# Kernel tuning notes

Measured on AMD Instinct MI355X. Metric: run time of the kernel, lower is better.

Reference implementation:

```python
import jax, jax.numpy as jnp
import numpy as np

WS = 7      # window size
NH = 16     # num heads
DIM = 512
B, H, W = 128, 28, 28


def _relative_position_index(ws):
    coords = np.stack(np.meshgrid(np.arange(ws), np.arange(ws), indexing='ij'))  # [2,ws,ws]
    coords = coords.reshape(2, -1)                                               # [2,ws^2]
    rel = coords[:, :, None] - coords[:, None, :]                                # [2,ws^2,ws^2]
    rel = rel.transpose(1, 2, 0)
    rel[:, :, 0] += ws - 1
    rel[:, :, 1] += ws - 1
    rel[:, :, 0] *= 2 * ws - 1
    return rel.sum(-1).reshape(-1).astype(np.int32)                              # [ws^2*ws^2]


def setup_inputs() -> dict:
    key = jax.random.key(0)
    ks = jax.random.split(key, 6)
    x = jax.random.normal(ks[0], (B, H, W, DIM), dtype=jnp.float32)
    nW = (H // WS) * (W // WS)
    mask = jnp.zeros((nW, WS * WS, WS * WS), dtype=jnp.float32)  # shifted-window mask (zeros = no shift)
    w_qkv = jax.random.normal(ks[1], (DIM, 3 * DIM), dtype=jnp.float32) * (DIM ** -0.5)
    b_qkv = jnp.zeros((3 * DIM,), dtype=jnp.float32)
    bias_table = jax.random.normal(ks[2], ((2 * WS - 1) ** 2, NH), dtype=jnp.float32) * 0.02
    w_proj = jax.random.normal(ks[3], (DIM, DIM), dtype=jnp.float32) * (DIM ** -0.5)
    b_proj = jnp.zeros((DIM,), dtype=jnp.float32)
    rel_index = jnp.asarray(_relative_position_index(WS))
    return {"x": x, "mask": mask, "w_qkv": w_qkv, "b_qkv": b_qkv,
            "bias_table": bias_table, "w_proj": w_proj, "b_proj": b_proj,
            "rel_index": rel_index, "height": H, "width": W}


def reference(x, mask, w_qkv, b_qkv, bias_table, w_proj, b_proj, rel_index, height, width):
    Bc, Hc, Wc, C = x.shape
    ws, nh = WS, NH
    hd = C // nh
    scale = hd ** -0.5
    hW, wW = height // ws, width // ws
    nW = hW * wW
    L = ws * ws

    # QKV projection: [B,H,W,3C]
    qkv = x @ w_qkv + b_qkv
    # fused window partition -> [3, B*nW, nh, ws^2, hd]
    qkv = qkv.reshape(Bc, hW, ws, wW, ws, 3, nh, hd)
    qkv = qkv.transpose(5, 0, 1, 3, 6, 2, 4, 7).reshape(3, Bc * nW, nh, L, hd)
    q, k, v = qkv[0], qkv[1], qkv[2]

    # scaled dot-product scores per window
    attn = jnp.einsum('wnqd,wnkd->wnqk', q * scale, k)  # [B*nW, nh, L, L]
    # relative position bias gather: [L*L, nh] -> [nh, L, L]
    bias = bias_table[rel_index].reshape(L, L, nh).transpose(2, 0, 1)
    attn = attn + bias[None]
    # shifted-window attention mask
    attn = attn.reshape(Bc, nW, nh, L, L) + mask[None, :, None]
    attn = jax.nn.softmax(attn, axis=-1).reshape(Bc * nW, nh, L, L)

    out = jnp.einsum('wnqk,wnkd->wnqd', attn, v)  # [B*nW, nh, L, hd]
    # fused window reverse -> [B,H,W,C]
    out = out.reshape(Bc, hW, wW, nh, ws, ws, hd)
    out = out.transpose(0, 1, 4, 2, 5, 3, 6).reshape(Bc, height, width, C)
    return out @ w_proj + b_proj
```

## Files before the change

### kernel.cpp

```cpp
#include <hip/hip_runtime.h>
#include <hip/hip_bf16.h>
#include <stdint.h>

typedef __bf16 bf16_t;
typedef bf16_t bf16x8 __attribute__((ext_vector_type(8)));
typedef float f32x4 __attribute__((ext_vector_type(4)));

#define MFMA16(a, b, c) __builtin_amdgcn_mfma_f32_16x16x32_bf16(a, b, c, 0, 0, 0)

static constexpr float kScale = 0.17677669529663687f;
static constexpr int CROWS = 25088;
static constexpr int NCHUNK = 4;

__device__ __forceinline__ void gload16(const bf16_t* g, bf16_t* l) {
  __builtin_amdgcn_global_load_lds(
      (const __attribute__((address_space(1))) unsigned int*)g,
      (__attribute__((address_space(3))) unsigned int*)l, 16, 0, 0);
}

__global__ __launch_bounds__(256) void k_prep(
    const float* __restrict__ wqkv,
    const float* __restrict__ wproj,
    const float* __restrict__ btab,
    const float* __restrict__ mask,
    const int*   __restrict__ relidx,
    bf16_t* __restrict__ wqkvT,
    bf16_t* __restrict__ wprojT,
    float*  __restrict__ bmm)
{
  int idx = blockIdx.x * 256 + threadIdx.x;
  if (idx < 1536 * 512) {
    int n = idx >> 9, k = idx & 511;
    wqkvT[idx] = (bf16_t)wqkv[k * 1536 + n];
  } else if (idx < 1536 * 512 + 512 * 512) {
    int t = idx - 1536 * 512;
    int n = t >> 9, k = t & 511;
    wprojT[t] = (bf16_t)wproj[k * 512 + n];
  } else if (idx < 1536 * 512 + 512 * 512 + 16 * 16 * 49 * 49) {
    int t = idx - (1536 * 512 + 512 * 512);
    int j = t % 49;  int t2 = t / 49;
    int i = t2 % 49; int t3 = t2 / 49;
    int h = t3 & 15; int wi = t3 >> 4;
    bmm[t] = btab[relidx[i * 49 + j] * 16 + h] + mask[(wi * 49 + i) * 49 + j];
  }
}

__global__ __launch_bounds__(256) void k_cvt(
    const float* __restrict__ x, bf16_t* __restrict__ xb)
{
  size_t i = (size_t)(blockIdx.x * 256 + threadIdx.x) * 8;
  float4 f0 = *(const float4*)(x + i);
  float4 f1 = *(const float4*)(x + i + 4);
  bf16x8 v;
  v[0] = (bf16_t)f0.x; v[1] = (bf16_t)f0.y; v[2] = (bf16_t)f0.z; v[3] = (bf16_t)f0.w;
  v[4] = (bf16_t)f1.x; v[5] = (bf16_t)f1.y; v[6] = (bf16_t)f1.z; v[7] = (bf16_t)f1.w;
  *(bf16x8*)(xb + i) = v;
}

template<int LDA, int NLD, bool ISQKV>
__global__ __launch_bounds__(256) void k_gemm(
    const bf16_t* __restrict__ A,
    const bf16_t* __restrict__ Bmat,
    const float*  __restrict__ bias,
    bf16_t* __restrict__ outb,
    float*  __restrict__ outf)
{
  __shared__ alignas(16) bf16_t As[128 * 64];
  __shared__ alignas(16) bf16_t Bs[128 * 64];
  const int tid  = threadIdx.x;
  const int wv   = tid >> 6, lane = tid & 63;
  const int quad = lane >> 4, l16 = lane & 15;
  const int nt0 = blockIdx.x * 128, mt0 = blockIdx.y * 128;
  const int wr = (wv >> 1) * 64, wc = (wv & 1) * 64;

  const int rsub = lane >> 3;
  const int colp = ((lane & 7) ^ rsub) * 8;
  const bf16_t* ga = A    + (size_t)(mt0 + wv * 32 + rsub) * LDA + colp;
  const bf16_t* gb = Bmat + (size_t)(nt0 + wv * 32 + rsub) * 512 + colp;
  bf16_t* lA = As + wv * 32 * 64;
  bf16_t* lB = Bs + wv * 32 * 64;

  const f32x4 z4 = {0.f, 0.f, 0.f, 0.f};
  f32x4 acc[4][4];
#pragma unroll
  for (int a = 0; a < 4; ++a)
#pragma unroll
    for (int b = 0; b < 4; ++b) acc[a][b] = z4;

  for (int kt = 0; kt < 8; ++kt) {
    const int k0 = kt * 64;
#pragma unroll
    for (int c = 0; c < 4; ++c) {
      gload16(ga + (size_t)c * 8 * LDA + k0, lA + c * 512);
      gload16(gb + c * 8 * 512 + k0, lB + c * 512);
    }
    __syncthreads();
#pragma unroll
    for (int kk = 0; kk < 2; ++kk) {
      bf16x8 af[4], bfr[4];
#pragma unroll
      for (int mt = 0; mt < 4; ++mt) {
        int row = wr + mt * 16 + l16;
        af[mt] = *(const bf16x8*)&As[row * 64 + ((kk * 32 + quad * 8) ^ ((l16 & 7) * 8))];
      }
#pragma unroll
      for (int nt = 0; nt < 4; ++nt) {
        int row = wc + nt * 16 + l16;
        bfr[nt] = *(const bf16x8*)&Bs[row * 64 + ((kk * 32 + quad * 8) ^ ((l16 & 7) * 8))];
      }
#pragma unroll
      for (int mt = 0; mt < 4; ++mt)
#pragma unroll
        for (int nt = 0; nt < 4; ++nt)
          acc[mt][nt] = MFMA16(af[mt], bfr[nt], acc[mt][nt]);
    }
    __syncthreads();
  }

#pragma unroll
  for (int nt = 0; nt < 4; ++nt) {
    int col = nt0 + wc + nt * 16 + l16;
    float bv = bias[col];
#pragma unroll
    for (int mt = 0; mt < 4; ++mt) {
#pragma unroll
      for (int r = 0; r < 4; ++r) {
        size_t row = (size_t)(mt0 + wr + mt * 16 + quad * 4 + r);
        float v = acc[mt][nt][r] + bv;
        if constexpr (ISQKV) {
          if (col < 512) v *= kScale;
          outb[row * NLD + col] = (bf16_t)v;
        } else {
          outf[row * NLD + col] = v;
        }
      }
    }
  }
}

__global__ __launch_bounds__(256) void k_attn2(
    bf16_t* __restrict__ qkv,
    const float* __restrict__ bmm)
{
  __shared__ alignas(16) bf16_t lds[4 * 6144];
  const int tid  = threadIdx.x;
  const int wv   = tid >> 6, lane = tid & 63;
  const int quad = lane >> 4, l16 = lane & 15;
  const int h = blockIdx.x * 4 + wv;
  const int w = blockIdx.y;
  const int bimg = w >> 4, wi = w & 15;
  const int rowbase = bimg * 784 + (wi >> 2) * 196 + (wi & 3) * 7;
  char* ps  = (char*)(lds + wv * 6144);
  char* vts = (char*)(lds + wv * 6144 + 4096);

  for (int u = lane; u < 32 * 16; u += 64) {
    int d = u >> 4, j = 48 + (u & 15);
    *(bf16_t*)(vts + ((d * 128 + j * 2) ^ ((d & 7) << 4))) = (bf16_t)0.f;
  }
  const bf16_t* vbase = qkv + 1024 + h * 32;
  for (int u = lane; u < 49 * 4; u += 64) {
    int l = u >> 2, dg = u & 3;
    size_t r = (size_t)(rowbase + (l / 7) * 28 + (l % 7));
    bf16x8 vvv = *(const bf16x8*)(vbase + r * 1536 + dg * 8);
#pragma unroll
    for (int e = 0; e < 8; ++e) {
      int d = dg * 8 + e;
      *(bf16_t*)(vts + ((d * 128 + l * 2) ^ ((d & 7) << 4))) = vvv[e];
    }
  }

  const bf16_t* qbase = qkv + h * 32;
  const bf16_t* kbase = qkv + 512 + h * 32;
  const f32x4 z4 = {0.f, 0.f, 0.f, 0.f};
  f32x4 sacc[4][4];
#pragma unroll
  for (int a = 0; a < 4; ++a)
#pragma unroll
    for (int b = 0; b < 4; ++b) sacc[a][b] = z4;

  bf16x8 kb[4];
#pragma unroll
  for (int nt = 0; nt < 4; ++nt) {
    int t = nt * 16 + l16; if (t > 48) t = 48;
    size_t r = (size_t)(rowbase + (t / 7) * 28 + (t % 7));
    kb[nt] = *(const bf16x8*)(kbase + r * 1536 + quad * 8);
  }
#pragma unroll
  for (int mt = 0; mt < 4; ++mt) {
    int t = mt * 16 + l16; if (t > 48) t = 48;
    size_t r = (size_t)(rowbase + (t / 7) * 28 + (t % 7));
    bf16x8 qa = *(const bf16x8*)(qbase + r * 1536 + quad * 8);
#pragma unroll
    for (int nt = 0; nt < 4; ++nt) sacc[mt][nt] = MFMA16(qa, kb[nt], sacc[mt][nt]);
  }

  const float* bm = bmm + (wi * 16 + h) * 2401;
#pragma unroll
  for (int mt = 0; mt < 4; ++mt) {
#pragma unroll
    for (int rr = 0; rr < 4; ++rr) {
      int i = mt * 16 + quad * 4 + rr;
      bool iv = (i < 49);
      float sv[4], mx = -3e38f;
#pragma unroll
      for (int nt = 0; nt < 4; ++nt) {
        int j = nt * 16 + l16;
        sv[nt] = (iv && j < 49) ? (sacc[mt][nt][rr] + bm[i * 49 + j]) : -3e38f;
        mx = fmaxf(mx, sv[nt]);
      }
#pragma unroll
      for (int off = 1; off < 16; off <<= 1) mx = fmaxf(mx, __shfl_xor(mx, off, 16));
      float ex[4], sum = 0.f;
#pragma unroll
      for (int nt = 0; nt < 4; ++nt) {
        ex[nt] = (sv[nt] > -2e38f) ? __expf(sv[nt] - mx) : 0.f;
        sum += ex[nt];
      }
#pragma unroll
      for (int off = 1; off < 16; off <<= 1) sum += __shfl_xor(sum, off, 16);
      float rinv = (sum > 0.f) ? (1.f / sum) : 0.f;
#pragma unroll
      for (int nt = 0; nt < 4; ++nt) {
        int j = nt * 16 + l16;
        *(bf16_t*)(ps + ((i * 128 + j * 2) ^ ((i & 7) << 4))) = (bf16_t)(ex[nt] * rinv);
      }
    }
  }

  asm volatile("" ::: "memory");

  f32x4 oacc[4][2];
#pragma unroll
  for (int a = 0; a < 4; ++a) { oacc[a][0] = z4; oacc[a][1] = z4; }
#pragma unroll
  for (int kk = 0; kk < 2; ++kk) {
    bf16x8 vb[2];
#pragma unroll
    for (int nt = 0; nt < 2; ++nt) {
      int d = nt * 16 + l16;
      vb[nt] = *(const bf16x8*)(vts + ((d * 128 + (kk * 32 + quad * 8) * 2) ^ ((d & 7) << 4)));
    }
#pragma unroll
    for (int mt = 0; mt < 4; ++mt) {
      int i = mt * 16 + l16;
      bf16x8 pa = *(const bf16x8*)(ps + ((i * 128 + (kk * 32 + quad * 8) * 2) ^ ((i & 7) << 4)));
#pragma unroll
      for (int nt = 0; nt < 2; ++nt) oacc[mt][nt] = MFMA16(pa, vb[nt], oacc[mt][nt]);
    }
  }

  bf16_t* obase = qkv + h * 32;
#pragma unroll
  for (int mt = 0; mt < 4; ++mt) {
#pragma unroll
    for (int rr = 0; rr < 4; ++rr) {
      int l = mt * 16 + quad * 4 + rr;
      if (l < 49) {
        size_t r = (size_t)(rowbase + (l / 7) * 28 + (l % 7));
#pragma unroll
        for (int nt = 0; nt < 2; ++nt)
          obase[r * 1536 + nt * 16 + l16] = (bf16_t)oacc[mt][nt][rr];
      }
    }
  }
}

extern "C" void kernel_launch(void* const* d_in, const int* in_sizes, int n_in,
                              void* d_out, int out_size, void* d_ws, size_t ws_size,
                              hipStream_t stream) {
  const float* x     = (const float*)d_in[0];
  const float* mask  = (const float*)d_in[1];
  const float* wqkv  = (const float*)d_in[2];
  const float* bqkv  = (const float*)d_in[3];
  const float* btab  = (const float*)d_in[4];
  const float* wproj = (const float*)d_in[5];
  const float* bproj = (const float*)d_in[6];
  const int*   relix = (const int*)d_in[7];
  float* out = (float*)d_out;

  char* ws = (char*)d_ws;
  bf16_t* wqkvT  = (bf16_t*)(ws);
  bf16_t* wprojT = (bf16_t*)(ws + 1572864);
  float*  bmm    = (float*)(ws + 2097152);
  bf16_t* xb     = (bf16_t*)(ws + 4555776);
  bf16_t* qkv    = (bf16_t*)(ws + 30245888);

  k_prep<<<6497, 256, 0, stream>>>(wqkv, wproj, btab, mask, relix, wqkvT, wprojT, bmm);
  for (int c = 0; c < NCHUNK; ++c) {
    const float* xc = x + (size_t)c * CROWS * 512;
    k_cvt<<<6272, 256, 0, stream>>>(xc, xb);
    k_gemm<512, 1536, true><<<dim3(12, 196), 256, 0, stream>>>(xb, wqkvT, bqkv, qkv, nullptr);
    k_attn2<<<dim3(4, 512), 256, 0, stream>>>(qkv, bmm);
    k_gemm<1536, 512, false><<<dim3(4, 196), 256, 0, stream>>>(qkv, wprojT, bproj, nullptr,
                                                               out + (size_t)c * CROWS * 512);
  }
}
```

Measured before the change: 866.4 us.

## Fuse fp32-to-bf16 conversion into QKV GEMM and pick chunk count from workspace size

Removes the separate x conversion kernel: the QKV GEMM now loads fp32 activations directly, converts them in registers and writes swizzled bf16 tiles to LDS, while weights still use async global-to-LDS loads. The chunk count now depends on workspace size, so the whole batch can run in a single pass of three launches instead of four chunks. Grid dimensions are swapped so row tiles vary fastest, which changes block ordering and weight-tile reuse in cache. The A-operand path now uses synchronous register loads, which may expose global latency inside the K loop.

```diff
diff --git a/kernel.cpp b/kernel.cpp
--- a/kernel.cpp
+++ b/kernel.cpp
@@ -9,8 +9,6 @@
 #define MFMA16(a, b, c) __builtin_amdgcn_mfma_f32_16x16x32_bf16(a, b, c, 0, 0, 0)
 
 static constexpr float kScale = 0.17677669529663687f;
-static constexpr int CROWS = 25088;
-static constexpr int NCHUNK = 4;
 
 __device__ __forceinline__ void gload16(const bf16_t* g, bf16_t* l) {
   __builtin_amdgcn_global_load_lds(
@@ -45,40 +43,27 @@
   }
 }
 
-__global__ __launch_bounds__(256) void k_cvt(
-    const float* __restrict__ x, bf16_t* __restrict__ xb)
-{
-  size_t i = (size_t)(blockIdx.x * 256 + threadIdx.x) * 8;
-  float4 f0 = *(const float4*)(x + i);
-  float4 f1 = *(const float4*)(x + i + 4);
-  bf16x8 v;
-  v[0] = (bf16_t)f0.x; v[1] = (bf16_t)f0.y; v[2] = (bf16_t)f0.z; v[3] = (bf16_t)f0.w;
-  v[4] = (bf16_t)f1.x; v[5] = (bf16_t)f1.y; v[6] = (bf16_t)f1.z; v[7] = (bf16_t)f1.w;
-  *(bf16x8*)(xb + i) = v;
-}
-
-template<int LDA, int NLD, bool ISQKV>
-__global__ __launch_bounds__(256) void k_gemm(
-    const bf16_t* __restrict__ A,
-    const bf16_t* __restrict__ Bmat,
+__global__ __launch_bounds__(256) void k_qkv(
+    const float*  __restrict__ X,
+    const bf16_t* __restrict__ Bw,
     const float*  __restrict__ bias,
-    bf16_t* __restrict__ outb,
-    float*  __restrict__ outf)
+    bf16_t* __restrict__ outq)
 {
   __shared__ alignas(16) bf16_t As[128 * 64];
   __shared__ alignas(16) bf16_t Bs[128 * 64];
   const int tid  = threadIdx.x;
   const int wv   = tid >> 6, lane = tid & 63;
   const int quad = lane >> 4, l16 = lane & 15;
-  const int nt0 = blockIdx.x * 128, mt0 = blockIdx.y * 128;
+  const int mt0 = blockIdx.x * 128, nt0 = blockIdx.y * 128;
   const int wr = (wv >> 1) * 64, wc = (wv & 1) * 64;
 
   const int rsub = lane >> 3;
   const int colp = ((lane & 7) ^ rsub) * 8;
-  const bf16_t* ga = A    + (size_t)(mt0 + wv * 32 + rsub) * LDA + colp;
-  const bf16_t* gb = Bmat + (size_t)(nt0 + wv * 32 + rsub) * 512 + colp;
-  bf16_t* lA = As + wv * 32 * 64;
-  bf16_t* lB = Bs + wv * 32 * 64;
+  const bf16_t* gb = Bw + (size_t)(nt0 + wv * 32 + rsub) * 512 + colp;
+  bf16_t* lB = Bs + wv * 2048;
+
+  const int arow = tid >> 3, acg = tid & 7;
+  const float* ga = X + (size_t)(mt0 + arow) * 512 + acg * 8;
 
   const f32x4 z4 = {0.f, 0.f, 0.f, 0.f};
   f32x4 acc[4][4];
@@ -90,24 +75,30 @@
   for (int kt = 0; kt < 8; ++kt) {
     const int k0 = kt * 64;
 #pragma unroll
-    for (int c = 0; c < 4; ++c) {
-      gload16(ga + (size_t)c * 8 * LDA + k0, lA + c * 512);
-      gload16(gb + c * 8 * 512 + k0, lB + c * 512);
+    for (int c = 0; c < 4; ++c)
+      gload16(gb + (size_t)c * 8 * 512 + k0, lB + c * 512);
+#pragma unroll
+    for (int s = 0; s < 4; ++s) {
+      const float* p = ga + (size_t)(s * 32) * 512 + k0;
+      float4 f0 = *(const float4*)p;
+      float4 f1 = *(const float4*)(p + 4);
+      int row = s * 32 + arow;
+      bf16x8 v;
+      v[0] = (bf16_t)f0.x; v[1] = (bf16_t)f0.y; v[2] = (bf16_t)f0.z; v[3] = (bf16_t)f0.w;
+      v[4] = (bf16_t)f1.x; v[5] = (bf16_t)f1.y; v[6] = (bf16_t)f1.z; v[7] = (bf16_t)f1.w;
+      *(bf16x8*)&As[row * 64 + ((acg * 8) ^ ((row & 7) * 8))] = v;
     }
     __syncthreads();
 #pragma unroll
     for (int kk = 0; kk < 2; ++kk) {
+      const int sw = (kk * 32 + quad * 8) ^ ((l16 & 7) * 8);
       bf16x8 af[4], bfr[4];
 #pragma unroll
-      for (int mt = 0; mt < 4; ++mt) {
-        int row = wr + mt * 16 + l16;
-        af[mt] = *(const bf16x8*)&As[row * 64 + ((kk * 32 + quad * 8) ^ ((l16 & 7) * 8))];
-      }
-#pragma unroll
-      for (int nt = 0; nt < 4; ++nt) {
-        int row = wc + nt * 16 + l16;
-        bfr[nt] = *(const bf16x8*)&Bs[row * 64 + ((kk * 32 + quad * 8) ^ ((l16 & 7) * 8))];
-      }
+      for (int mt = 0; mt < 4; ++mt)
+        af[mt] = *(const bf16x8*)&As[(wr + mt * 16 + l16) * 64 + sw];
+#pragma unroll
+      for (int nt = 0; nt < 4; ++nt)
+        bfr[nt] = *(const bf16x8*)&Bs[(wc + nt * 16 + l16) * 64 + sw];
 #pragma unroll
       for (int mt = 0; mt < 4; ++mt)
 #pragma unroll
@@ -127,12 +118,78 @@
       for (int r = 0; r < 4; ++r) {
         size_t row = (size_t)(mt0 + wr + mt * 16 + quad * 4 + r);
         float v = acc[mt][nt][r] + bv;
-        if constexpr (ISQKV) {
-          if (col < 512) v *= kScale;
-          outb[row * NLD + col] = (bf16_t)v;
-        } else {
-          outf[row * NLD + col] = v;
-        }
+        if (col < 512) v *= kScale;
+        outq[row * 1536 + col] = (bf16_t)v;
+      }
+    }
+  }
+}
+
+__global__ __launch_bounds__(256) void k_proj(
+    const bf16_t* __restrict__ Aq,
+    const bf16_t* __restrict__ Bw,
+    const float*  __restrict__ bias,
+    float* __restrict__ out)
+{
+  __shared__ alignas(16) bf16_t As[128 * 64];
+  __shared__ alignas(16) bf16_t Bs[128 * 64];
+  const int tid  = threadIdx.x;
+  const int wv   = tid >> 6, lane = tid & 63;
+  const int quad = lane >> 4, l16 = lane & 15;
+  const int mt0 = blockIdx.x * 128, nt0 = blockIdx.y * 128;
+  const int wr = (wv >> 1) * 64, wc = (wv & 1) * 64;
+
+  const int rsub = lane >> 3;
+  const int colp = ((lane & 7) ^ rsub) * 8;
+  const bf16_t* ga = Aq + (size_t)(mt0 + wv * 32 + rsub) * 1536 + colp;
+  const bf16_t* gb = Bw + (size_t)(nt0 + wv * 32 + rsub) * 512 + colp;
+  bf16_t* lA = As + wv * 2048;
+  bf16_t* lB = Bs + wv * 2048;
+
+  const f32x4 z4 = {0.f, 0.f, 0.f, 0.f};
+  f32x4 acc[4][4];
+#pragma unroll
+  for (int a = 0; a < 4; ++a)
+#pragma unroll
+    for (int b = 0; b < 4; ++b) acc[a][b] = z4;
+
+  for (int kt = 0; kt < 8; ++kt) {
+    const int k0 = kt * 64;
+#pragma unroll
+    for (int c = 0; c < 4; ++c) {
+      gload16(ga + (size_t)c * 8 * 1536 + k0, lA + c * 512);
+      gload16(gb + (size_t)c * 8 * 512 + k0, lB + c * 512);
+    }
+    __syncthreads();
+#pragma unroll
+    for (int kk = 0; kk < 2; ++kk) {
+      const int sw = (kk * 32 + quad * 8) ^ ((l16 & 7) * 8);
+      bf16x8 af[4], bfr[4];
+#pragma unroll
+      for (int mt = 0; mt < 4; ++mt)
+        af[mt] = *(const bf16x8*)&As[(wr + mt * 16 + l16) * 64 + sw];
+#pragma unroll
+      for (int nt = 0; nt < 4; ++nt)
+        bfr[nt] = *(const bf16x8*)&Bs[(wc + nt * 16 + l16) * 64 + sw];
+#pragma unroll
+      for (int mt = 0; mt < 4; ++mt)
+#pragma unroll
+        for (int nt = 0; nt < 4; ++nt)
+          acc[mt][nt] = MFMA16(af[mt], bfr[nt], acc[mt][nt]);
+    }
+    __syncthreads();
+  }
+
+#pragma unroll
+  for (int nt = 0; nt < 4; ++nt) {
+    int col = nt0 + wc + nt * 16 + l16;
+    float bv = bias[col];
+#pragma unroll
+    for (int mt = 0; mt < 4; ++mt) {
+#pragma unroll
+      for (int r = 0; r < 4; ++r) {
+        size_t row = (size_t)(mt0 + wr + mt * 16 + quad * 4 + r);
+        out[row * 512 + col] = acc[mt][nt][r] + bv;
       }
     }
   }
@@ -146,8 +203,8 @@
   const int tid  = threadIdx.x;
   const int wv   = tid >> 6, lane = tid & 63;
   const int quad = lane >> 4, l16 = lane & 15;
-  const int h = blockIdx.x * 4 + wv;
-  const int w = blockIdx.y;
+  const int h = blockIdx.y * 4 + wv;
+  const int w = blockIdx.x;
   const int bimg = w >> 4, wi = w & 15;
   const int rowbase = bimg * 784 + (wi >> 2) * 196 + (wi & 3) * 7;
   char* ps  = (char*)(lds + wv * 6144);
@@ -282,16 +339,20 @@
   bf16_t* wqkvT  = (bf16_t*)(ws);
   bf16_t* wprojT = (bf16_t*)(ws + 1572864);
   float*  bmm    = (float*)(ws + 2097152);
-  bf16_t* xb     = (bf16_t*)(ws + 4555776);
-  bf16_t* qkv    = (bf16_t*)(ws + 30245888);
+  bf16_t* qkv    = (bf16_t*)(ws + 4555776);
+
+  int nchunk = 1;
+  if (ws_size < 4555776ull + 100352ull * 3072ull) nchunk = 2;
+  if (ws_size < 4555776ull + 50176ull * 3072ull)  nchunk = 4;
+  const int rows = 100352 / nchunk;
+  const int nimg = 128 / nchunk;
 
   k_prep<<<6497, 256, 0, stream>>>(wqkv, wproj, btab, mask, relix, wqkvT, wprojT, bmm);
-  for (int c = 0; c < NCHUNK; ++c) {
-    const float* xc = x + (size_t)c * CROWS * 512;
-    k_cvt<<<6272, 256, 0, stream>>>(xc, xb);
-    k_gemm<512, 1536, true><<<dim3(12, 196), 256, 0, stream>>>(xb, wqkvT, bqkv, qkv, nullptr);
-    k_attn2<<<dim3(4, 512), 256, 0, stream>>>(qkv, bmm);
-    k_gemm<1536, 512, false><<<dim3(4, 196), 256, 0, stream>>>(qkv, wprojT, bproj, nullptr,
-                                                               out + (size_t)c * CROWS * 512);
-  }
-}
+  for (int c = 0; c < nchunk; ++c) {
+    const float* xc = x + (size_t)c * rows * 512;
+    k_qkv<<<dim3(rows / 128, 12), 256, 0, stream>>>(xc, wqkvT, bqkv, qkv);
+    k_attn2<<<dim3(nimg * 16, 4), 256, 0, stream>>>(qkv, bmm);
+    k_proj<<<dim3(rows / 128, 4), 256, 0, stream>>>(qkv, wprojT, bproj,
+                                                    out + (size_t)c * rows * 512);
+  }
+}
```

Result: slower. 987.0 us (+13.9%).

## Choose chunk count from workspace size to cut kernel launches

Applied to the files above, without the earlier changes.

Picks the number of row chunks (1, 2 or 4) from the available workspace size, so a large workspace runs the whole batch in one pass rather than four. The conversion kernel becomes grid-stride with an explicit element count, and the attention grid is transposed so windows lie along x. Fewer chunks means fewer launches and larger GEMM grids that fill the GPU better, at the cost of a larger qkv intermediate that may fall out of cache. The swizzle offset in the GEMM is also hoisted out of the inner load loops.

```diff
diff --git a/kernel.cpp b/kernel.cpp
--- a/kernel.cpp
+++ b/kernel.cpp
@@ -9,8 +9,6 @@
 #define MFMA16(a, b, c) __builtin_amdgcn_mfma_f32_16x16x32_bf16(a, b, c, 0, 0, 0)
 
 static constexpr float kScale = 0.17677669529663687f;
-static constexpr int CROWS = 25088;
-static constexpr int NCHUNK = 4;
 
 __device__ __forceinline__ void gload16(const bf16_t* g, bf16_t* l) {
   __builtin_amdgcn_global_load_lds(
@@ -46,15 +44,18 @@
 }
 
 __global__ __launch_bounds__(256) void k_cvt(
-    const float* __restrict__ x, bf16_t* __restrict__ xb)
+    const float* __restrict__ x, bf16_t* __restrict__ xb, int count)
 {
-  size_t i = (size_t)(blockIdx.x * 256 + threadIdx.x) * 8;
-  float4 f0 = *(const float4*)(x + i);
-  float4 f1 = *(const float4*)(x + i + 4);
-  bf16x8 v;
-  v[0] = (bf16_t)f0.x; v[1] = (bf16_t)f0.y; v[2] = (bf16_t)f0.z; v[3] = (bf16_t)f0.w;
-  v[4] = (bf16_t)f1.x; v[5] = (bf16_t)f1.y; v[6] = (bf16_t)f1.z; v[7] = (bf16_t)f1.w;
-  *(bf16x8*)(xb + i) = v;
+  for (size_t i = blockIdx.x * 256 + threadIdx.x; i < (size_t)count;
+       i += (size_t)gridDim.x * 256) {
+    size_t o = i * 8;
+    float4 f0 = *(const float4*)(x + o);
+    float4 f1 = *(const float4*)(x + o + 4);
+    bf16x8 v;
+    v[0] = (bf16_t)f0.x; v[1] = (bf16_t)f0.y; v[2] = (bf16_t)f0.z; v[3] = (bf16_t)f0.w;
+    v[4] = (bf16_t)f1.x; v[5] = (bf16_t)f1.y; v[6] = (bf16_t)f1.z; v[7] = (bf16_t)f1.w;
+    *(bf16x8*)(xb + o) = v;
+  }
 }
 
 template<int LDA, int NLD, bool ISQKV>
@@ -97,17 +98,14 @@
     __syncthreads();
 #pragma unroll
     for (int kk = 0; kk < 2; ++kk) {
+      const int sw = (kk * 32 + quad * 8) ^ ((l16 & 7) * 8);
       bf16x8 af[4], bfr[4];
 #pragma unroll
-      for (int mt = 0; mt < 4; ++mt) {
-        int row = wr + mt * 16 + l16;
-        af[mt] = *(const bf16x8*)&As[row * 64 + ((kk * 32 + quad * 8) ^ ((l16 & 7) * 8))];
-      }
-#pragma unroll
-      for (int nt = 0; nt < 4; ++nt) {
-        int row = wc + nt * 16 + l16;
-        bfr[nt] = *(const bf16x8*)&Bs[row * 64 + ((kk * 32 + quad * 8) ^ ((l16 & 7) * 8))];
-      }
+      for (int mt = 0; mt < 4; ++mt)
+        af[mt] = *(const bf16x8*)&As[(wr + mt * 16 + l16) * 64 + sw];
+#pragma unroll
+      for (int nt = 0; nt < 4; ++nt)
+        bfr[nt] = *(const bf16x8*)&Bs[(wc + nt * 16 + l16) * 64 + sw];
 #pragma unroll
       for (int mt = 0; mt < 4; ++mt)
 #pragma unroll
@@ -146,8 +144,8 @@
   const int tid  = threadIdx.x;
   const int wv   = tid >> 6, lane = tid & 63;
   const int quad = lane >> 4, l16 = lane & 15;
-  const int h = blockIdx.x * 4 + wv;
-  const int w = blockIdx.y;
+  const int h = blockIdx.y * 4 + wv;
+  const int w = blockIdx.x;
   const int bimg = w >> 4, wi = w & 15;
   const int rowbase = bimg * 784 + (wi >> 2) * 196 + (wi & 3) * 7;
   char* ps  = (char*)(lds + wv * 6144);
@@ -278,20 +276,26 @@
   const int*   relix = (const int*)d_in[7];
   float* out = (float*)d_out;
 
+  int nchunk = 1;
+  if (ws_size < 415597568ull) nchunk = 2;
+  if (ws_size < 210076672ull) nchunk = 4;
+  const int rows = 100352 / nchunk;
+  const int nimg = 128 / nchunk;
+
   char* ws = (char*)d_ws;
   bf16_t* wqkvT  = (bf16_t*)(ws);
   bf16_t* wprojT = (bf16_t*)(ws + 1572864);
   float*  bmm    = (float*)(ws + 2097152);
   bf16_t* xb     = (bf16_t*)(ws + 4555776);
-  bf16_t* qkv    = (bf16_t*)(ws + 30245888);
+  bf16_t* qkv    = (bf16_t*)(ws + 4555776 + (size_t)rows * 1024);
 
   k_prep<<<6497, 256, 0, stream>>>(wqkv, wproj, btab, mask, relix, wqkvT, wprojT, bmm);
-  for (int c = 0; c < NCHUNK; ++c) {
-    const float* xc = x + (size_t)c * CROWS * 512;
-    k_cvt<<<6272, 256, 0, stream>>>(xc, xb);
-    k_gemm<512, 1536, true><<<dim3(12, 196), 256, 0, stream>>>(xb, wqkvT, bqkv, qkv, nullptr);
-    k_attn2<<<dim3(4, 512), 256, 0, stream>>>(qkv, bmm);
-    k_gemm<1536, 512, false><<<dim3(4, 196), 256, 0, stream>>>(qkv, wprojT, bproj, nullptr,
-                                                               out + (size_t)c * CROWS * 512);
-  }
-}
+  for (int c = 0; c < nchunk; ++c) {
+    const float* xc = x + (size_t)c * rows * 512;
+    k_cvt<<<4096, 256, 0, stream>>>(xc, xb, rows * 64);
+    k_gemm<512, 1536, true><<<dim3(12, rows / 128), 256, 0, stream>>>(xb, wqkvT, bqkv, qkv, nullptr);
+    k_attn2<<<dim3(nimg * 16, 4), 256, 0, stream>>>(qkv, bmm);
+    k_gemm<1536, 512, false><<<dim3(4, rows / 128), 256, 0, stream>>>(qkv, wprojT, bproj, nullptr,
+                                                                      out + (size_t)c * rows * 512);
+  }
+}
```

Result: slower. 935.9 us (+8.0%).
